# Kernel optimization log

Hardware: AMD Instinct MI355X
Metric: run time of the kernel (lower is better)

The kernel has to match this reference:

```python
import jax, jax.numpy as jnp
import numpy as np
from jax import lax

# --- configuration (matches init_kwargs) ---
NY_I = NX_I = 256      # interior model size
PML = 20               # pml width on each edge
DX = 4.0               # grid spacing (m)
DT = 5e-4              # time step (s); CFL: vmax*DT/DX ~ 0.4 < 0.5
NT = 64                # number of time steps
C1, C2 = 9.0 / 8.0, -1.0 / 24.0   # 4th-order staggered FD coefficients


def _shift(p, axis, off, n):
    idx = [slice(None)] * 3
    idx[axis] = slice(2 + off, 2 + off + n)
    return p[tuple(idx)]


def _dfwd(f, axis):
    # forward (half-cell +) staggered derivative, 4th order, zero halo
    pad = [(0, 0)] * 3
    pad[axis] = (2, 2)
    p = jnp.pad(f, pad)
    n = f.shape[axis]
    return (C1 * (_shift(p, axis, 1, n) - _shift(p, axis, 0, n))
            + C2 * (_shift(p, axis, 2, n) - _shift(p, axis, -1, n))) / DX


def _dbwd(f, axis):
    # backward (half-cell -) staggered derivative, 4th order, zero halo
    pad = [(0, 0)] * 3
    pad[axis] = (2, 2)
    p = jnp.pad(f, pad)
    n = f.shape[axis]
    return (C1 * (_shift(p, axis, 0, n) - _shift(p, axis, -1, n))
            + C2 * (_shift(p, axis, 1, n) - _shift(p, axis, -2, n))) / DX


def _propagate(lamb, mu, buoyancy, amps, src_loc, rec_loc):
    # replicate model edges into the PML region (as deepwave does)
    lambp = jnp.pad(lamb, PML, mode='edge')[None]      # [1,NY,NX]
    mup = jnp.pad(mu, PML, mode='edge')[None]
    buoyp = jnp.pad(buoyancy, PML, mode='edge')[None]
    NY, NX = lambp.shape[1], lambp.shape[2]
    n_shots = amps.shape[0]
    l2m = lambp + 2.0 * mup

    # CPML damping profiles (quadratic), alpha=0, kappa=1
    max_vel = lax.stop_gradient(jnp.max(jnp.sqrt(l2m * buoyp)))
    sig_max = 3.0 * max_vel * jnp.log(1000.0) / (2.0 * PML * DX)

    def prof(n):
        i = jnp.arange(n, dtype=lamb.dtype)
        d = jnp.maximum(jnp.clip(PML - i, 0.0, None),
                        jnp.clip(i - (n - 1 - PML), 0.0, None)) / PML
        return sig_max * d * d

    by = jnp.exp(-prof(NY) * DT)[None, :, None]
    ay = by - 1.0
    bx = jnp.exp(-prof(NX) * DT)[None, None, :]
    ax = bx - 1.0

    shot = jnp.arange(n_shots)[:, None]
    sl = src_loc + PML   # [S,nsrc,2]
    rl = rec_loc + PML   # [S,nrec,2]
    src_b = buoyp[0, sl[..., 0], sl[..., 1]]   # buoyancy at sources [S,nsrc]

    z = jnp.zeros((n_shots, NY, NX), lamb.dtype)
    carry0 = (z,) * 13  # vy,vx,syy,sxy,sxx, m_vyy,m_vyx,m_vxy,m_vxx, m_syyy,m_sxyy,m_sxyx,m_sxxx

    def step(carry, amp_t):
        (vy, vx, syy, sxy, sxx,
         mvyy, mvyx, mvxy, mvxx,
         msyyy, msxyy, msxyx, msxxx) = carry
        # --- velocity update ---
        d = _dbwd(syy, 1); msyyy = by * msyyy + ay * d; dsyy_y = d + msyyy
        d = _dbwd(sxy, 2); msxyx = bx * msxyx + ax * d; dsxy_x = d + msxyx
        vy = vy + DT * buoyp * (dsyy_y + dsxy_x)
        d = _dbwd(sxy, 1); msxyy = by * msxyy + ay * d; dsxy_y = d + msxyy
        d = _dbwd(sxx, 2); msxxx = bx * msxxx + ax * d; dsxx_x = d + msxxx
        vx = vx + DT * buoyp * (dsxy_y + dsxx_x)
        # --- inject y-oriented sources into vy ---
        vy = vy.at[shot, sl[..., 0], sl[..., 1]].add(DT * src_b * amp_t)
        # --- stress update ---
        d = _dfwd(vy, 1); mvyy = by * mvyy + ay * d; dvy_y = d + mvyy
        d = _dfwd(vx, 2); mvxx = bx * mvxx + ax * d; dvx_x = d + mvxx
        syy = syy + DT * (l2m * dvy_y + lambp * dvx_x)
        sxx = sxx + DT * (lambp * dvy_y + l2m * dvx_x)
        d = _dfwd(vy, 2); mvyx = bx * mvyx + ax * d; dvy_x = d + mvyx
        d = _dfwd(vx, 1); mvxy = by * mvxy + ay * d; dvx_y = d + mvxy
        sxy = sxy + DT * mup * (dvy_x + dvx_y)
        # --- record y-oriented receivers ---
        rec = vy[shot, rl[..., 0], rl[..., 1]]   # [S,nrec]
        return ((vy, vx, syy, sxy, sxx,
                 mvyy, mvyx, mvxy, mvxx,
                 msyyy, msxyy, msxyx, msxxx), rec)

    _, recs = lax.scan(step, carry0, jnp.moveaxis(amps, 2, 0))  # recs [nt,S,nrec]
    return jnp.transpose(recs, (1, 2, 0))  # [S,nrec,nt]


def setup_inputs() -> dict:
    key = jax.random.key(0)
    k = jax.random.split(key, 6)
    vp = 3000.0 + 100.0 * jax.random.normal(k[0], (NY_I, NX_I), jnp.float32)
    vs = 1500.0 + 50.0 * jax.random.normal(k[1], (NY_I, NX_I), jnp.float32)
    rho = 2200.0 + 50.0 * jax.random.normal(k[2], (NY_I, NX_I), jnp.float32)
    mu = rho * vs ** 2
    lamb = rho * (vp ** 2 - 2.0 * vs ** 2)
    buoyancy = 1.0 / rho
    source_amplitudes_y = jax.random.normal(k[3], (2, 8, NT), jnp.float32)
    source_locations_y = jax.random.randint(k[4], (2, 8, 2), 0, NY_I)
    receiver_locations_y = jax.random.randint(k[5], (2, 64, 2), 0, NY_I)
    return {
        'lamb': lamb, 'mu': mu, 'buoyancy': buoyancy,
        'source_amplitudes_y': source_amplitudes_y,
        'source_locations_y': source_locations_y,
        'receiver_locations_y': receiver_locations_y,
    }


def reference(lamb, mu, buoyancy, source_amplitudes_y,
              source_locations_y, receiver_locations_y):
    return _propagate(lamb, mu, buoyancy, source_amplitudes_y,
                      source_locations_y, receiver_locations_y)
```

## Files before the change

### kernel.cpp

```cpp
#include <hip/hip_runtime.h>
#include <math.h>

static constexpr int NYI  = 256;
static constexpr int PMLW = 20;
static constexpr int NY   = 296, NX = 296;
static constexpr int NCELL = NY * NX;
static constexpr int NS   = 2;
static constexpr int NSRC = 8;
static constexpr int NREC = 64;
static constexpr int NT   = 64;
static constexpr float DXF = 4.0f;
static constexpr float DTF = 5e-4f;
static constexpr float FC1 = 9.0f / 8.0f;
static constexpr float FC2 = -1.0f / 24.0f;
static constexpr float INV_DX = 1.0f / DXF;

static constexpr int TB = 8, TS = 37;
static constexpr int VS = TS + 4;
static constexpr int SS = TS + 8;
static constexpr int NBLK = TB * TB * NS;
static constexpr int NTHR = 512;
static constexpr int VAREA = VS * VS;
static constexpr int TAREA = TS * TS;
static constexpr int SFRAME = SS * SS - TAREA;
static constexpr int KV = 4, KT = 3;

static constexpr int GSLOT   = 3 * NS * NCELL;
static constexpr int FLG_OFF = 2 * GSLOT;

__device__ __forceinline__ float cohload(const float* p) {
    return __hip_atomic_load(p, __ATOMIC_RELAXED, __HIP_MEMORY_SCOPE_AGENT);
}
__device__ __forceinline__ void cohstore(float* p, float v) {
    __hip_atomic_store(p, v, __ATOMIC_RELAXED, __HIP_MEMORY_SCOPE_AGENT);
}

__global__ __launch_bounds__(NTHR, 1)
void elastic_fused(const float* __restrict__ lamb, const float* __restrict__ mu,
                   const float* __restrict__ buoy, const float* __restrict__ amps,
                   const int* __restrict__ src_loc, const int* __restrict__ rec_loc,
                   float* __restrict__ out, float* __restrict__ ws)
{
    __shared__ float sS[3][SS * SS];
    __shared__ float sV[2][VS * VS];
    __shared__ float byt[VS], ayt[VS], bxt[VS], axt[VS];
    __shared__ float sAmp[NSRC * NT];
    __shared__ float wmax[NTHR / 64];
    __shared__ int   rcnt;
    __shared__ short rl_r[NREC];
    __shared__ int   rl_pos[NREC];

    int* flags = (int*)(ws + FLG_OFF);
    unsigned* gvm = (unsigned*)(flags + NBLK);
    float* gstr = ws;

    const int tid  = threadIdx.x;
    const int shot = blockIdx.x & 1;
    const int tb   = blockIdx.x >> 1;
    const int bty  = tb >> 3, btx = tb & 7;
    const int gy0  = bty * TS, gx0 = btx * TS;
    const int myBlk = blockIdx.x;

    int myNbr = -1;
    if (tid < 8) {
        int idx = tid < 4 ? tid : tid + 1;
        int dy = idx / 3 - 1, dx = idx % 3 - 1;
        int nty = bty + dy, ntx = btx + dx;
        if (nty >= 0 && nty < TB && ntx >= 0 && ntx < TB)
            myNbr = ((nty * TB + ntx) << 1) | shot;
    }

    for (int i = tid; i < 3 * SS * SS; i += NTHR) ((float*)sS)[i] = 0.0f;
    for (int i = tid; i < 2 * VS * VS; i += NTHR) ((float*)sV)[i] = 0.0f;
    if (tid == 0) rcnt = 0;

    {
        int i = myBlk * NTHR + tid;
        float v = (lamb[i] + 2.0f * mu[i]) * buoy[i];
        #pragma unroll
        for (int off = 32; off > 0; off >>= 1)
            v = fmaxf(v, __shfl_down(v, off));
        if ((tid & 63) == 0) wmax[tid >> 6] = v;
    }

    int   sidx_v[KV], vyv[KV], vxv[KV], smk[KV];
    float buo_v[KV];
    float msyyy[KV] = {0,0,0,0}, msxyx[KV] = {0,0,0,0};
    float msxyy[KV] = {0,0,0,0}, msxxx[KV] = {0,0,0,0};
    unsigned cvm = 0, intm = 0;
    #pragma unroll
    for (int k = 0; k < KV; ++k) {
        int vi = tid + NTHR * k;
        bool val = vi < VAREA;
        int vy_ = val ? vi / VS : 0;
        int vx_ = val ? vi - vy_ * VS : 0;
        int gy = gy0 - 2 + vy_, gx = gx0 - 2 + vx_;
        bool ing = val && gy >= 0 && gy < NY && gx >= 0 && gx < NX;
        if (ing) cvm |= 1u << k;
        if (ing && vy_ >= 4 && vy_ <= 37 && vx_ >= 4 && vx_ <= 37) intm |= 1u << k;
        vyv[k] = vy_; vxv[k] = vx_;
        sidx_v[k] = (vy_ + 2) * SS + (vx_ + 2);
        float b = 0.0f;
        if (ing) {
            int iy = min(max(gy - PMLW, 0), NYI - 1);
            int ix = min(max(gx - PMLW, 0), NYI - 1);
            b = buoy[iy * NYI + ix];
        }
        buo_v[k] = b;
        int sm = 0;
        #pragma unroll
        for (int s = 0; s < NSRC; ++s) {
            int sy = src_loc[(shot * NSRC + s) * 2 + 0] + PMLW;
            int sx = src_loc[(shot * NSRC + s) * 2 + 1] + PMLW;
            if (ing && sy == gy && sx == gx) sm |= 1 << s;
        }
        smk[k] = sm;
    }
    const unsigned bndm = cvm & ~intm;

    int   sidx_t[KT], vidx_t[KT], gidx_t[KT], tyt[KT], txt[KT];
    float lam_t[KT], mu_t[KT], l2m_t[KT];
    float mvyy[KT] = {0,0,0}, mvxx[KT] = {0,0,0}, mvyx[KT] = {0,0,0}, mvxy[KT] = {0,0,0};
    unsigned ctm = 0, ringm = 0;
    #pragma unroll
    for (int k = 0; k < KT; ++k) {
        int ti = tid + NTHR * k;
        bool val = ti < TAREA;
        int ty = val ? ti / TS : 0;
        int tx = val ? ti - ty * TS : 0;
        int gy = gy0 + ty, gx = gx0 + tx;
        if (val) ctm |= 1u << k;
        if (val && (ty < 4 || ty >= TS - 4 || tx < 4 || tx >= TS - 4)) ringm |= 1u << k;
        tyt[k] = ty; txt[k] = tx;
        sidx_t[k] = (ty + 4) * SS + (tx + 4);
        vidx_t[k] = (ty + 2) * VS + (tx + 2);
        gidx_t[k] = gy * NX + gx;
        float la = 0.0f, m = 0.0f;
        if (val) {
            int iy = min(max(gy - PMLW, 0), NYI - 1);
            int ix = min(max(gx - PMLW, 0), NYI - 1);
            la = lamb[iy * NYI + ix];
            m  = mu  [iy * NYI + ix];
        }
        lam_t[k] = la; mu_t[k] = m; l2m_t[k] = la + 2.0f * m;
    }

    bool fval[2], fin[2];
    int  flidx[2], fgi[2];
    #pragma unroll
    for (int k = 0; k < 2; ++k) {
        int ff = tid + NTHR * k;
        fval[k] = ff < SFRAME;
        int fy = 0, fx = 0;
        if (fval[k]) {
            if (ff < 4 * SS)      { fy = ff / SS;                 fx = ff - fy * SS; }
            else if (ff < 8 * SS) { int r = ff - 4 * SS; fy = SS - 4 + r / SS; fx = r % SS; }
            else {
                int r = ff - 8 * SS;
                if (r < (SS - 8) * 4) { fy = 4 + (r >> 2); fx = r & 3; }
                else { r -= (SS - 8) * 4; fy = 4 + (r >> 2); fx = SS - 4 + (r & 3); }
            }
        }
        int gy = gy0 - 4 + fy, gx = gx0 - 4 + fx;
        fin[k]   = fval[k] && gy >= 0 && gy < NY && gx >= 0 && gx < NX;
        flidx[k] = fy * SS + fx;
        fgi[k]   = fin[k] ? (gy * NX + gx) : 0;
    }

    __syncthreads();

    if (tid == 0) {
        float v = wmax[0];
        #pragma unroll
        for (int w = 1; w < NTHR / 64; ++w) v = fmaxf(v, wmax[w]);
        __hip_atomic_store(&gvm[myBlk], __float_as_uint(v), __ATOMIC_RELAXED,
                           __HIP_MEMORY_SCOPE_AGENT);
    }
    unsigned* sred = (unsigned*)sAmp;
    if (tid < NBLK) {
        unsigned v;
        for (;;) {
            v = __hip_atomic_load(&gvm[tid], __ATOMIC_RELAXED, __HIP_MEMORY_SCOPE_AGENT);
            if (!(v & 0x80000000u)) break;
            __builtin_amdgcn_s_sleep(1);
        }
        sred[tid] = v;
    }
    __syncthreads();
    if (tid == 0) {
        unsigned mb = sred[0];
        for (int i = 1; i < NBLK; ++i) mb = mb > sred[i] ? mb : sred[i];
        wmax[0] = __uint_as_float(mb);
    }
    __syncthreads();

    const float max_vel = sqrtf(wmax[0]);
    const float sig_max = 3.0f * max_vel * logf(1000.0f) / (2.0f * PMLW * DXF);
    if (tid < VS) {
        auto prof = [&](int g) -> float {
            float fi = (float)g;
            float d1 = fmaxf((float)PMLW - fi, 0.0f);
            float d2 = fmaxf(fi - (float)(NY - 1 - PMLW), 0.0f);
            float dd = fmaxf(d1, d2) * (1.0f / (float)PMLW);
            return expf(-(sig_max * dd * dd) * DTF);
        };
        float b = prof(gy0 - 2 + tid); byt[tid] = b; ayt[tid] = b - 1.0f;
        b = prof(gx0 - 2 + tid);       bxt[tid] = b; axt[tid] = b - 1.0f;
    }
    if (tid < NREC) {
        int r = tid;
        int ry = rec_loc[(shot * NREC + r) * 2 + 0] + PMLW;
        int rx = rec_loc[(shot * NREC + r) * 2 + 1] + PMLW;
        if (ry >= gy0 && ry < gy0 + TS && rx >= gx0 && rx < gx0 + TS) {
            int p = atomicAdd(&rcnt, 1);
            rl_r[p]   = (short)r;
            rl_pos[p] = (ry - gy0 + 2) * VS + (rx - gx0 + 2);
        }
    }
    __syncthreads();
    for (int i = tid; i < NSRC * NT; i += NTHR)
        sAmp[i] = amps[shot * NSRC * NT + i];
    __syncthreads();

    auto do_vel = [&](unsigned m, int t) {
        #pragma unroll
        for (int k = 0; k < KV; ++k) {
            if (!((m >> k) & 1)) continue;
            int si = sidx_v[k];
            float by_ = byt[vyv[k]], ay_ = ayt[vyv[k]];
            float bx_ = bxt[vxv[k]], ax_ = axt[vxv[k]];
            float d, mm;
            d = (FC1 * (sS[0][si] - sS[0][si - SS]) + FC2 * (sS[0][si + SS] - sS[0][si - 2 * SS])) * INV_DX;
            mm = by_ * msyyy[k] + ay_ * d;  msyyy[k] = mm;  float dsyy_y = d + mm;
            d = (FC1 * (sS[1][si] - sS[1][si - 1]) + FC2 * (sS[1][si + 1] - sS[1][si - 2])) * INV_DX;
            mm = bx_ * msxyx[k] + ax_ * d;  msxyx[k] = mm;  float dsxy_x = d + mm;
            d = (FC1 * (sS[1][si] - sS[1][si - SS]) + FC2 * (sS[1][si + SS] - sS[1][si - 2 * SS])) * INV_DX;
            mm = by_ * msxyy[k] + ay_ * d;  msxyy[k] = mm;  float dsxy_y = d + mm;
            d = (FC1 * (sS[2][si] - sS[2][si - 1]) + FC2 * (sS[2][si + 1] - sS[2][si - 2])) * INV_DX;
            mm = bx_ * msxxx[k] + ax_ * d;  msxxx[k] = mm;  float dsxx_x = d + mm;
            int vi = tid + NTHR * k;
            float nvy = sV[0][vi] + DTF * buo_v[k] * (dsyy_y + dsxy_x);
            float nvx = sV[1][vi] + DTF * buo_v[k] * (dsxy_y + dsxx_x);
            if (smk[k]) {
                #pragma unroll
                for (int s = 0; s < NSRC; ++s)
                    if ((smk[k] >> s) & 1) nvy += DTF * buo_v[k] * sAmp[s * NT + t];
            }
            sV[0][vi] = nvy;
            sV[1][vi] = nvx;
        }
    };

    auto do_stress = [&](unsigned m, bool pub, float* gsw) {
        #pragma unroll
        for (int k = 0; k < KT; ++k) {
            if (!((m >> k) & 1)) continue;
            int si = sidx_t[k], vi = vidx_t[k];
            float by_ = byt[tyt[k] + 2], ay_ = ayt[tyt[k] + 2];
            float bx_ = bxt[txt[k] + 2], ax_ = axt[txt[k] + 2];
            float d, mm;
            d = (FC1 * (sV[0][vi + VS] - sV[0][vi]) + FC2 * (sV[0][vi + 2 * VS] - sV[0][vi - VS])) * INV_DX;
            mm = by_ * mvyy[k] + ay_ * d;  mvyy[k] = mm;  float dvy_y = d + mm;
            d = (FC1 * (sV[1][vi + 1] - sV[1][vi]) + FC2 * (sV[1][vi + 2] - sV[1][vi - 1])) * INV_DX;
            mm = bx_ * mvxx[k] + ax_ * d;  mvxx[k] = mm;  float dvx_x = d + mm;
            float nsyy = sS[0][si] + DTF * (l2m_t[k] * dvy_y + lam_t[k] * dvx_x);
            float nsxx = sS[2][si] + DTF * (lam_t[k] * dvy_y + l2m_t[k] * dvx_x);
            d = (FC1 * (sV[0][vi + 1] - sV[0][vi]) + FC2 * (sV[0][vi + 2] - sV[0][vi - 1])) * INV_DX;
            mm = bx_ * mvyx[k] + ax_ * d;  mvyx[k] = mm;  float dvy_x = d + mm;
            d = (FC1 * (sV[1][vi + VS] - sV[1][vi]) + FC2 * (sV[1][vi + 2 * VS] - sV[1][vi - VS])) * INV_DX;
            mm = by_ * mvxy[k] + ay_ * d;  mvxy[k] = mm;  float dvx_y = d + mm;
            float nsxy = sS[1][si] + DTF * mu_t[k] * (dvy_x + dvx_y);
            sS[0][si] = nsyy; sS[1][si] = nsxy; sS[2][si] = nsxx;
            if (pub && ((ringm >> k) & 1)) {
                int gi = gidx_t[k];
                cohstore(&gsw[(0 * NS + shot) * NCELL + gi], nsyy);
                cohstore(&gsw[(1 * NS + shot) * NCELL + gi], nsxy);
                cohstore(&gsw[(2 * NS + shot) * NCELL + gi], nsxx);
            }
        }
    };

    for (int t = 0; t < NT; ++t) {
        const float* gsr = gstr + ((t + 1) & 1) * GSLOT;
        float*       gsw = gstr + (t & 1) * GSLOT;

        do_vel(intm, t);

        if (t > 0 && myNbr >= 0) {
            while (__hip_atomic_load(&flags[myNbr], __ATOMIC_RELAXED,
                                     __HIP_MEMORY_SCOPE_AGENT) < t)
                __builtin_amdgcn_s_sleep(1);
        }
        __syncthreads();

        float fr0[3], fr1[3];
        #pragma unroll
        for (int f = 0; f < 3; ++f) {
            fr0[f] = (t > 0 && fin[0]) ? cohload(&gsr[(f * NS + shot) * NCELL + fgi[0]]) : 0.0f;
            fr1[f] = (t > 0 && fin[1]) ? cohload(&gsr[(f * NS + shot) * NCELL + fgi[1]]) : 0.0f;
        }

        do_stress(ctm & ~ringm, false, gsw);

        if (fval[0]) { sS[0][flidx[0]] = fr0[0]; sS[1][flidx[0]] = fr0[1]; sS[2][flidx[0]] = fr0[2]; }
        if (fval[1]) { sS[0][flidx[1]] = fr1[0]; sS[1][flidx[1]] = fr1[1]; sS[2][flidx[1]] = fr1[2]; }
        __syncthreads();

        do_vel(bndm, t);
        __syncthreads();

        if (tid < rcnt)
            out[(shot * NREC + rl_r[tid]) * NT + t] = sV[0][rl_pos[tid]];

        do_stress(ringm, true, gsw);

        __syncthreads();
        if (tid == 0 && t < NT - 1)
            __hip_atomic_store(&flags[myBlk], t + 1, __ATOMIC_RELAXED,
                               __HIP_MEMORY_SCOPE_AGENT);
    }
}

extern "C" void kernel_launch(void* const* d_in, const int* in_sizes, int n_in,
                              void* d_out, int out_size, void* d_ws, size_t ws_size,
                              hipStream_t stream) {
    const float* lamb    = (const float*)d_in[0];
    const float* mu      = (const float*)d_in[1];
    const float* buoy    = (const float*)d_in[2];
    const float* amps    = (const float*)d_in[3];
    const int*   src_loc = (const int*)d_in[4];
    const int*   rec_loc = (const int*)d_in[5];
    float* ws  = (float*)d_ws;
    float* out = (float*)d_out;

    elastic_fused<<<NBLK, NTHR, 0, stream>>>(lamb, mu, buoy, amps, src_loc, rec_loc, out, ws);
}
```

Before: 330.1 us.

## Split domain into 8x16 rectangular tiles to double persistent block count

```diff
diff --git a/kernel.cpp b/kernel.cpp
--- a/kernel.cpp
+++ b/kernel.cpp
@@ -15,15 +15,17 @@
 static constexpr float FC2 = -1.0f / 24.0f;
 static constexpr float INV_DX = 1.0f / DXF;
 
-static constexpr int TB = 8, TS = 37;
-static constexpr int VS = TS + 4;
-static constexpr int SS = TS + 8;
-static constexpr int NBLK = TB * TB * NS;
+static constexpr int TBY = 8, TBX = 16;
+static constexpr int TSY = 37, TSX = 19;
+static constexpr int VSY = TSY + 4, VSX = TSX + 4;
+static constexpr int SSY = TSY + 8, SSX = TSX + 8;
+static constexpr int VAREA = VSY * VSX;
+static constexpr int SAREA = SSY * SSX;
+static constexpr int TAREA = TSY * TSX;
+static constexpr int SFRAME = SAREA - TAREA;
+static constexpr int NBLK = TBX * TBY * NS;
 static constexpr int NTHR = 512;
-static constexpr int VAREA = VS * VS;
-static constexpr int TAREA = TS * TS;
-static constexpr int SFRAME = SS * SS - TAREA;
-static constexpr int KV = 4, KT = 3;
+static constexpr int KV = 2, KT = 2;
 
 static constexpr int GSLOT   = 3 * NS * NCELL;
 static constexpr int FLG_OFF = 2 * GSLOT;
@@ -41,9 +43,9 @@
                    const int* __restrict__ src_loc, const int* __restrict__ rec_loc,
                    float* __restrict__ out, float* __restrict__ ws)
 {
-    __shared__ float sS[3][SS * SS];
-    __shared__ float sV[2][VS * VS];
-    __shared__ float byt[VS], ayt[VS], bxt[VS], axt[VS];
+    __shared__ float sS[3][SAREA];
+    __shared__ float sV[2][VAREA];
+    __shared__ float byt[VSY], ayt[VSY], bxt[VSX], axt[VSX];
     __shared__ float sAmp[NSRC * NT];
     __shared__ float wmax[NTHR / 64];
     __shared__ int   rcnt;
@@ -57,8 +59,8 @@
     const int tid  = threadIdx.x;
     const int shot = blockIdx.x & 1;
     const int tb   = blockIdx.x >> 1;
-    const int bty  = tb >> 3, btx = tb & 7;
-    const int gy0  = bty * TS, gx0 = btx * TS;
+    const int bty  = tb >> 4, btx = tb & 15;
+    const int gy0  = bty * TSY, gx0 = btx * TSX;
     const int myBlk = blockIdx.x;
 
     int myNbr = -1;
@@ -66,17 +68,20 @@
         int idx = tid < 4 ? tid : tid + 1;
         int dy = idx / 3 - 1, dx = idx % 3 - 1;
         int nty = bty + dy, ntx = btx + dx;
-        if (nty >= 0 && nty < TB && ntx >= 0 && ntx < TB)
-            myNbr = ((nty * TB + ntx) << 1) | shot;
-    }
-
-    for (int i = tid; i < 3 * SS * SS; i += NTHR) ((float*)sS)[i] = 0.0f;
-    for (int i = tid; i < 2 * VS * VS; i += NTHR) ((float*)sV)[i] = 0.0f;
+        if (nty >= 0 && nty < TBY && ntx >= 0 && ntx < TBX)
+            myNbr = ((nty * TBX + ntx) << 1) | shot;
+    }
+
+    for (int i = tid; i < 3 * SAREA; i += NTHR) ((float*)sS)[i] = 0.0f;
+    for (int i = tid; i < 2 * VAREA; i += NTHR) ((float*)sV)[i] = 0.0f;
     if (tid == 0) rcnt = 0;
 
     {
-        int i = myBlk * NTHR + tid;
-        float v = (lamb[i] + 2.0f * mu[i]) * buoy[i];
+        float v = 0.0f;
+        if (tid < 256) {
+            int i = myBlk * 256 + tid;
+            v = (lamb[i] + 2.0f * mu[i]) * buoy[i];
+        }
         #pragma unroll
         for (int off = 32; off > 0; off >>= 1)
             v = fmaxf(v, __shfl_down(v, off));
@@ -85,21 +90,21 @@
 
     int   sidx_v[KV], vyv[KV], vxv[KV], smk[KV];
     float buo_v[KV];
-    float msyyy[KV] = {0,0,0,0}, msxyx[KV] = {0,0,0,0};
-    float msxyy[KV] = {0,0,0,0}, msxxx[KV] = {0,0,0,0};
+    float msyyy[KV] = {0,0}, msxyx[KV] = {0,0};
+    float msxyy[KV] = {0,0}, msxxx[KV] = {0,0};
     unsigned cvm = 0, intm = 0;
     #pragma unroll
     for (int k = 0; k < KV; ++k) {
         int vi = tid + NTHR * k;
         bool val = vi < VAREA;
-        int vy_ = val ? vi / VS : 0;
-        int vx_ = val ? vi - vy_ * VS : 0;
+        int vy_ = val ? vi / VSX : 0;
+        int vx_ = val ? vi - vy_ * VSX : 0;
         int gy = gy0 - 2 + vy_, gx = gx0 - 2 + vx_;
         bool ing = val && gy >= 0 && gy < NY && gx >= 0 && gx < NX;
         if (ing) cvm |= 1u << k;
-        if (ing && vy_ >= 4 && vy_ <= 37 && vx_ >= 4 && vx_ <= 37) intm |= 1u << k;
+        if (ing && vy_ >= 4 && vy_ <= TSY && vx_ >= 4 && vx_ <= TSX) intm |= 1u << k;
         vyv[k] = vy_; vxv[k] = vx_;
-        sidx_v[k] = (vy_ + 2) * SS + (vx_ + 2);
+        sidx_v[k] = (vy_ + 2) * SSX + (vx_ + 2);
         float b = 0.0f;
         if (ing) {
             int iy = min(max(gy - PMLW, 0), NYI - 1);
@@ -120,20 +125,21 @@
 
     int   sidx_t[KT], vidx_t[KT], gidx_t[KT], tyt[KT], txt[KT];
     float lam_t[KT], mu_t[KT], l2m_t[KT];
-    float mvyy[KT] = {0,0,0}, mvxx[KT] = {0,0,0}, mvyx[KT] = {0,0,0}, mvxy[KT] = {0,0,0};
+    float mvyy[KT] = {0,0}, mvxx[KT] = {0,0}, mvyx[KT] = {0,0}, mvxy[KT] = {0,0};
     unsigned ctm = 0, ringm = 0;
     #pragma unroll
     for (int k = 0; k < KT; ++k) {
         int ti = tid + NTHR * k;
-        bool val = ti < TAREA;
-        int ty = val ? ti / TS : 0;
-        int tx = val ? ti - ty * TS : 0;
+        bool v0 = ti < TAREA;
+        int ty = v0 ? ti / TSX : 0;
+        int tx = v0 ? ti - ty * TSX : 0;
         int gy = gy0 + ty, gx = gx0 + tx;
+        bool val = v0 && gx < NX;
         if (val) ctm |= 1u << k;
-        if (val && (ty < 4 || ty >= TS - 4 || tx < 4 || tx >= TS - 4)) ringm |= 1u << k;
+        if (val && (ty < 4 || ty >= TSY - 4 || tx < 4 || tx >= TSX - 4)) ringm |= 1u << k;
         tyt[k] = ty; txt[k] = tx;
-        sidx_t[k] = (ty + 4) * SS + (tx + 4);
-        vidx_t[k] = (ty + 2) * VS + (tx + 2);
+        sidx_t[k] = (ty + 4) * SSX + (tx + 4);
+        vidx_t[k] = (ty + 2) * VSX + (tx + 2);
         gidx_t[k] = gy * NX + gx;
         float la = 0.0f, m = 0.0f;
         if (val) {
@@ -145,26 +151,23 @@
         lam_t[k] = la; mu_t[k] = m; l2m_t[k] = la + 2.0f * m;
     }
 
-    bool fval[2], fin[2];
-    int  flidx[2], fgi[2];
-    #pragma unroll
-    for (int k = 0; k < 2; ++k) {
-        int ff = tid + NTHR * k;
-        fval[k] = ff < SFRAME;
-        int fy = 0, fx = 0;
-        if (fval[k]) {
-            if (ff < 4 * SS)      { fy = ff / SS;                 fx = ff - fy * SS; }
-            else if (ff < 8 * SS) { int r = ff - 4 * SS; fy = SS - 4 + r / SS; fx = r % SS; }
-            else {
-                int r = ff - 8 * SS;
-                if (r < (SS - 8) * 4) { fy = 4 + (r >> 2); fx = r & 3; }
-                else { r -= (SS - 8) * 4; fy = 4 + (r >> 2); fx = SS - 4 + (r & 3); }
-            }
+    bool fin0;
+    int  flidx0, fgi0;
+    {
+        int ff = tid;
+        int fy, fx;
+        if (ff < 4 * SSX)       { fy = ff / SSX;                fx = ff - fy * SSX; }
+        else if (ff < 8 * SSX)  { int r = ff - 4 * SSX; fy = SSY - 4 + r / SSX; fx = r % SSX; }
+        else {
+            int r = ff - 8 * SSX;
+            fy = 4 + (r >> 3);
+            int c = r & 7;
+            fx = c < 4 ? c : (SSX - 8 + c);
         }
         int gy = gy0 - 4 + fy, gx = gx0 - 4 + fx;
-        fin[k]   = fval[k] && gy >= 0 && gy < NY && gx >= 0 && gx < NX;
-        flidx[k] = fy * SS + fx;
-        fgi[k]   = fin[k] ? (gy * NX + gx) : 0;
+        fin0   = gy >= 0 && gy < NY && gx >= 0 && gx < NX;
+        flidx0 = fy * SSX + fx;
+        fgi0   = fin0 ? (gy * NX + gx) : 0;
     }
 
     __syncthreads();
@@ -196,7 +199,7 @@
 
     const float max_vel = sqrtf(wmax[0]);
     const float sig_max = 3.0f * max_vel * logf(1000.0f) / (2.0f * PMLW * DXF);
-    if (tid < VS) {
+    {
         auto prof = [&](int g) -> float {
             float fi = (float)g;
             float d1 = fmaxf((float)PMLW - fi, 0.0f);
@@ -204,17 +207,21 @@
             float dd = fmaxf(d1, d2) * (1.0f / (float)PMLW);
             return expf(-(sig_max * dd * dd) * DTF);
         };
-        float b = prof(gy0 - 2 + tid); byt[tid] = b; ayt[tid] = b - 1.0f;
-        b = prof(gx0 - 2 + tid);       bxt[tid] = b; axt[tid] = b - 1.0f;
+        if (tid < VSY) {
+            float b = prof(gy0 - 2 + tid); byt[tid] = b; ayt[tid] = b - 1.0f;
+        }
+        if (tid < VSX) {
+            float b = prof(gx0 - 2 + tid); bxt[tid] = b; axt[tid] = b - 1.0f;
+        }
     }
     if (tid < NREC) {
         int r = tid;
         int ry = rec_loc[(shot * NREC + r) * 2 + 0] + PMLW;
         int rx = rec_loc[(shot * NREC + r) * 2 + 1] + PMLW;
-        if (ry >= gy0 && ry < gy0 + TS && rx >= gx0 && rx < gx0 + TS) {
+        if (ry >= gy0 && ry < gy0 + TSY && rx >= gx0 && rx < gx0 + TSX) {
             int p = atomicAdd(&rcnt, 1);
             rl_r[p]   = (short)r;
-            rl_pos[p] = (ry - gy0 + 2) * VS + (rx - gx0 + 2);
+            rl_pos[p] = (ry - gy0 + 2) * VSX + (rx - gx0 + 2);
         }
     }
     __syncthreads();
@@ -230,11 +237,11 @@
             float by_ = byt[vyv[k]], ay_ = ayt[vyv[k]];
             float bx_ = bxt[vxv[k]], ax_ = axt[vxv[k]];
             float d, mm;
-            d = (FC1 * (sS[0][si] - sS[0][si - SS]) + FC2 * (sS[0][si + SS] - sS[0][si - 2 * SS])) * INV_DX;
+            d = (FC1 * (sS[0][si] - sS[0][si - SSX]) + FC2 * (sS[0][si + SSX] - sS[0][si - 2 * SSX])) * INV_DX;
             mm = by_ * msyyy[k] + ay_ * d;  msyyy[k] = mm;  float dsyy_y = d + mm;
             d = (FC1 * (sS[1][si] - sS[1][si - 1]) + FC2 * (sS[1][si + 1] - sS[1][si - 2])) * INV_DX;
             mm = bx_ * msxyx[k] + ax_ * d;  msxyx[k] = mm;  float dsxy_x = d + mm;
-            d = (FC1 * (sS[1][si] - sS[1][si - SS]) + FC2 * (sS[1][si + SS] - sS[1][si - 2 * SS])) * INV_DX;
+            d = (FC1 * (sS[1][si] - sS[1][si - SSX]) + FC2 * (sS[1][si + SSX] - sS[1][si - 2 * SSX])) * INV_DX;
             mm = by_ * msxyy[k] + ay_ * d;  msxyy[k] = mm;  float dsxy_y = d + mm;
             d = (FC1 * (sS[2][si] - sS[2][si - 1]) + FC2 * (sS[2][si + 1] - sS[2][si - 2])) * INV_DX;
             mm = bx_ * msxxx[k] + ax_ * d;  msxxx[k] = mm;  float dsxx_x = d + mm;
@@ -259,7 +266,7 @@
             float by_ = byt[tyt[k] + 2], ay_ = ayt[tyt[k] + 2];
             float bx_ = bxt[txt[k] + 2], ax_ = axt[txt[k] + 2];
             float d, mm;
-            d = (FC1 * (sV[0][vi + VS] - sV[0][vi]) + FC2 * (sV[0][vi + 2 * VS] - sV[0][vi - VS])) * INV_DX;
+            d = (FC1 * (sV[0][vi + VSX] - sV[0][vi]) + FC2 * (sV[0][vi + 2 * VSX] - sV[0][vi - VSX])) * INV_DX;
             mm = by_ * mvyy[k] + ay_ * d;  mvyy[k] = mm;  float dvy_y = d + mm;
             d = (FC1 * (sV[1][vi + 1] - sV[1][vi]) + FC2 * (sV[1][vi + 2] - sV[1][vi - 1])) * INV_DX;
             mm = bx_ * mvxx[k] + ax_ * d;  mvxx[k] = mm;  float dvx_x = d + mm;
@@ -267,7 +274,7 @@
             float nsxx = sS[2][si] + DTF * (lam_t[k] * dvy_y + l2m_t[k] * dvx_x);
             d = (FC1 * (sV[0][vi + 1] - sV[0][vi]) + FC2 * (sV[0][vi + 2] - sV[0][vi - 1])) * INV_DX;
             mm = bx_ * mvyx[k] + ax_ * d;  mvyx[k] = mm;  float dvy_x = d + mm;
-            d = (FC1 * (sV[1][vi + VS] - sV[1][vi]) + FC2 * (sV[1][vi + 2 * VS] - sV[1][vi - VS])) * INV_DX;
+            d = (FC1 * (sV[1][vi + VSX] - sV[1][vi]) + FC2 * (sV[1][vi + 2 * VSX] - sV[1][vi - VSX])) * INV_DX;
             mm = by_ * mvxy[k] + ay_ * d;  mvxy[k] = mm;  float dvx_y = d + mm;
             float nsxy = sS[1][si] + DTF * mu_t[k] * (dvy_x + dvx_y);
             sS[0][si] = nsyy; sS[1][si] = nsxy; sS[2][si] = nsxx;
@@ -293,17 +300,14 @@
         }
         __syncthreads();
 
-        float fr0[3], fr1[3];
-        #pragma unroll
-        for (int f = 0; f < 3; ++f) {
-            fr0[f] = (t > 0 && fin[0]) ? cohload(&gsr[(f * NS + shot) * NCELL + fgi[0]]) : 0.0f;
-            fr1[f] = (t > 0 && fin[1]) ? cohload(&gsr[(f * NS + shot) * NCELL + fgi[1]]) : 0.0f;
-        }
+        float fr0[3];
+        #pragma unroll
+        for (int f = 0; f < 3; ++f)
+            fr0[f] = (t > 0 && fin0) ? cohload(&gsr[(f * NS + shot) * NCELL + fgi0]) : 0.0f;
 
         do_stress(ctm & ~ringm, false, gsw);
 
-        if (fval[0]) { sS[0][flidx[0]] = fr0[0]; sS[1][flidx[0]] = fr0[1]; sS[2][flidx[0]] = fr0[2]; }
-        if (fval[1]) { sS[0][flidx[1]] = fr1[0]; sS[1][flidx[1]] = fr1[1]; sS[2][flidx[1]] = fr1[2]; }
+        sS[0][flidx0] = fr0[0]; sS[1][flidx0] = fr0[1]; sS[2][flidx0] = fr0[2];
         __syncthreads();
 
         do_vel(bndm, t);
```

After: 389.7 us. +18.0%, slower.

## Compute four cells per thread with float4 LDS loads and padded tiles

Applied to the files above, without the earlier changes.

```diff
diff --git a/kernel.cpp b/kernel.cpp
--- a/kernel.cpp
+++ b/kernel.cpp
@@ -16,14 +16,13 @@
 static constexpr float INV_DX = 1.0f / DXF;
 
 static constexpr int TB = 8, TS = 37;
-static constexpr int VS = TS + 4;
-static constexpr int SS = TS + 8;
 static constexpr int NBLK = TB * TB * NS;
 static constexpr int NTHR = 512;
-static constexpr int VAREA = VS * VS;
-static constexpr int TAREA = TS * TS;
-static constexpr int SFRAME = SS * SS - TAREA;
-static constexpr int KV = 4, KT = 3;
+static constexpr int SVW = 44, VROWS = 41;
+static constexpr int SSW = 48, SROWS = 45;
+static constexpr int NVINT = 272, NVTOT = 451;
+static constexpr int NSEARLY = 217, NSTOT = 370;
+static constexpr int SFRAME = 656;
 
 static constexpr int GSLOT   = 3 * NS * NCELL;
 static constexpr int FLG_OFF = 2 * GSLOT;
@@ -35,15 +34,25 @@
     __hip_atomic_store(p, v, __ATOMIC_RELAXED, __HIP_MEMORY_SCOPE_AGENT);
 }
 
+__device__ __forceinline__ void ld8(float* __restrict__ dst,
+                                    const float* __restrict__ arr, int idx) {
+    float4 A_ = *(const float4*)&arr[idx];
+    float4 B_ = *(const float4*)&arr[idx + 4];
+    dst[0] = A_.x; dst[1] = A_.y; dst[2] = A_.z; dst[3] = A_.w;
+    dst[4] = B_.x; dst[5] = B_.y; dst[6] = B_.z; dst[7] = B_.w;
+}
+
 __global__ __launch_bounds__(NTHR, 1)
 void elastic_fused(const float* __restrict__ lamb, const float* __restrict__ mu,
                    const float* __restrict__ buoy, const float* __restrict__ amps,
                    const int* __restrict__ src_loc, const int* __restrict__ rec_loc,
                    float* __restrict__ out, float* __restrict__ ws)
 {
-    __shared__ float sS[3][SS * SS];
-    __shared__ float sV[2][VS * VS];
-    __shared__ float byt[VS], ayt[VS], bxt[VS], axt[VS];
+    __shared__ __align__(16) float sSyy[SROWS * SSW];
+    __shared__ __align__(16) float sSxy[SROWS * SSW];
+    __shared__ __align__(16) float sSxx[SROWS * SSW];
+    __shared__ __align__(16) float sVy[VROWS * SVW];
+    __shared__ __align__(16) float sVx[VROWS * SVW];
     __shared__ float sAmp[NSRC * NT];
     __shared__ float wmax[NTHR / 64];
     __shared__ int   rcnt;
@@ -70,8 +79,8 @@
             myNbr = ((nty * TB + ntx) << 1) | shot;
     }
 
-    for (int i = tid; i < 3 * SS * SS; i += NTHR) ((float*)sS)[i] = 0.0f;
-    for (int i = tid; i < 2 * VS * VS; i += NTHR) ((float*)sV)[i] = 0.0f;
+    for (int i = tid; i < SROWS * SSW; i += NTHR) { sSyy[i] = 0.0f; sSxy[i] = 0.0f; sSxx[i] = 0.0f; }
+    for (int i = tid; i < VROWS * SVW; i += NTHR) { sVy[i] = 0.0f; sVx[i] = 0.0f; }
     if (tid == 0) rcnt = 0;
 
     {
@@ -83,66 +92,78 @@
         if ((tid & 63) == 0) wmax[tid >> 6] = v;
     }
 
-    int   sidx_v[KV], vyv[KV], vxv[KV], smk[KV];
-    float buo_v[KV];
-    float msyyy[KV] = {0,0,0,0}, msxyx[KV] = {0,0,0,0};
-    float msxyy[KV] = {0,0,0,0}, msxxx[KV] = {0,0,0,0};
-    unsigned cvm = 0, intm = 0;
+    const bool vact = tid < NVTOT;
+    const bool vint = tid < NVINT;
+    int vrow = 0, vq = 0;
+    if (vint) { vrow = 4 + tid / 8; vq = 1 + (tid & 7); }
+    else if (vact) {
+        int j = tid - NVINT;
+        if (j < 44)      { vrow = j / 11; vq = j % 11; }
+        else if (j < 77) { int k = j - 44; vrow = 38 + k / 11; vq = k % 11; }
+        else             { int k = j - 77; vrow = 4 + k / 3; int c = k % 3;
+                           vq = (c == 0) ? 0 : (c == 1 ? 9 : 10); }
+    }
+    const int c0v = 4 * vq;
+    const int gyv = gy0 - 2 + vrow;
+
+    int sly[NSRC], slx[NSRC];
     #pragma unroll
-    for (int k = 0; k < KV; ++k) {
-        int vi = tid + NTHR * k;
-        bool val = vi < VAREA;
-        int vy_ = val ? vi / VS : 0;
-        int vx_ = val ? vi - vy_ * VS : 0;
-        int gy = gy0 - 2 + vy_, gx = gx0 - 2 + vx_;
-        bool ing = val && gy >= 0 && gy < NY && gx >= 0 && gx < NX;
-        if (ing) cvm |= 1u << k;
-        if (ing && vy_ >= 4 && vy_ <= 37 && vx_ >= 4 && vx_ <= 37) intm |= 1u << k;
-        vyv[k] = vy_; vxv[k] = vx_;
-        sidx_v[k] = (vy_ + 2) * SS + (vx_ + 2);
+    for (int s = 0; s < NSRC; ++s) {
+        sly[s] = src_loc[(shot * NSRC + s) * 2 + 0] + PMLW;
+        slx[s] = src_loc[(shot * NSRC + s) * 2 + 1] + PMLW;
+    }
+
+    int vdm = 0, smk4 = 0;
+    float buo[4];
+    #pragma unroll
+    for (int m = 0; m < 4; ++m) {
+        int vx_ = c0v + m;
+        int gx = gx0 - 2 + vx_;
+        bool ing = vact && vx_ <= 40 && gyv >= 0 && gyv < NY && gx >= 0 && gx < NX;
+        if (ing) vdm |= 1 << m;
         float b = 0.0f;
         if (ing) {
-            int iy = min(max(gy - PMLW, 0), NYI - 1);
+            int iy = min(max(gyv - PMLW, 0), NYI - 1);
             int ix = min(max(gx - PMLW, 0), NYI - 1);
             b = buoy[iy * NYI + ix];
         }
-        buo_v[k] = b;
-        int sm = 0;
-        #pragma unroll
-        for (int s = 0; s < NSRC; ++s) {
-            int sy = src_loc[(shot * NSRC + s) * 2 + 0] + PMLW;
-            int sx = src_loc[(shot * NSRC + s) * 2 + 1] + PMLW;
-            if (ing && sy == gy && sx == gx) sm |= 1 << s;
-        }
-        smk[k] = sm;
-    }
-    const unsigned bndm = cvm & ~intm;
-
-    int   sidx_t[KT], vidx_t[KT], gidx_t[KT], tyt[KT], txt[KT];
-    float lam_t[KT], mu_t[KT], l2m_t[KT];
-    float mvyy[KT] = {0,0,0}, mvxx[KT] = {0,0,0}, mvyx[KT] = {0,0,0}, mvxy[KT] = {0,0,0};
-    unsigned ctm = 0, ringm = 0;
+        buo[m] = b;
+        #pragma unroll
+        for (int s = 0; s < NSRC; ++s)
+            if (ing && sly[s] == gyv && slx[s] == gx) smk4 |= 1 << (m * 8 + s);
+    }
+
+    const bool sact = tid < NSTOT;
+    const bool searly = tid < NSEARLY;
+    int trow = 0, tq = 0;
+    if (searly) { trow = 3 + tid / 7; tq = 1 + tid % 7; }
+    else if (sact) {
+        int j = tid - NSEARLY;
+        if (j < 30)      { trow = j / 10; tq = j % 10; }
+        else if (j < 60) { int k = j - 30; trow = 34 + k / 10; tq = k % 10; }
+        else             { int k = j - 60; trow = 3 + k / 3; int c = k % 3;
+                           tq = (c == 0) ? 0 : (c == 1 ? 8 : 9); }
+    }
+    const int q0 = 4 * tq;
+    const int gys = gy0 + trow;
+    int tmask = 0, rmask = 0;
+    float lam[4], muv[4], l2m[4];
+    int gidx[4];
     #pragma unroll
-    for (int k = 0; k < KT; ++k) {
-        int ti = tid + NTHR * k;
-        bool val = ti < TAREA;
-        int ty = val ? ti / TS : 0;
-        int tx = val ? ti - ty * TS : 0;
-        int gy = gy0 + ty, gx = gx0 + tx;
-        if (val) ctm |= 1u << k;
-        if (val && (ty < 4 || ty >= TS - 4 || tx < 4 || tx >= TS - 4)) ringm |= 1u << k;
-        tyt[k] = ty; txt[k] = tx;
-        sidx_t[k] = (ty + 4) * SS + (tx + 4);
-        vidx_t[k] = (ty + 2) * VS + (tx + 2);
-        gidx_t[k] = gy * NX + gx;
-        float la = 0.0f, m = 0.0f;
+    for (int m = 0; m < 4; ++m) {
+        int tx = q0 + m;
+        bool val = sact && tx <= 36;
+        if (val) tmask |= 1 << m;
+        if (val && (trow < 4 || trow >= TS - 4 || tx < 4 || tx >= TS - 4)) rmask |= 1 << m;
+        gidx[m] = gys * NX + (gx0 + tx);
+        float la = 0.0f, mm_ = 0.0f;
         if (val) {
-            int iy = min(max(gy - PMLW, 0), NYI - 1);
-            int ix = min(max(gx - PMLW, 0), NYI - 1);
+            int iy = min(max(gys - PMLW, 0), NYI - 1);
+            int ix = min(max(gx0 + tx - PMLW, 0), NYI - 1);
             la = lamb[iy * NYI + ix];
-            m  = mu  [iy * NYI + ix];
-        }
-        lam_t[k] = la; mu_t[k] = m; l2m_t[k] = la + 2.0f * m;
+            mm_ = mu[iy * NYI + ix];
+        }
+        lam[m] = la; muv[m] = mm_; l2m[m] = la + 2.0f * mm_;
     }
 
     bool fval[2], fin[2];
@@ -153,17 +174,17 @@
         fval[k] = ff < SFRAME;
         int fy = 0, fx = 0;
         if (fval[k]) {
-            if (ff < 4 * SS)      { fy = ff / SS;                 fx = ff - fy * SS; }
-            else if (ff < 8 * SS) { int r = ff - 4 * SS; fy = SS - 4 + r / SS; fx = r % SS; }
+            if (ff < 4 * SROWS)      { fy = ff / SROWS; fx = ff - fy * SROWS; }
+            else if (ff < 8 * SROWS) { int r = ff - 4 * SROWS; fy = 41 + r / SROWS; fx = r % SROWS; }
             else {
-                int r = ff - 8 * SS;
-                if (r < (SS - 8) * 4) { fy = 4 + (r >> 2); fx = r & 3; }
-                else { r -= (SS - 8) * 4; fy = 4 + (r >> 2); fx = SS - 4 + (r & 3); }
+                int r = ff - 8 * SROWS;
+                if (r < 37 * 4) { fy = 4 + (r >> 2); fx = r & 3; }
+                else { r -= 37 * 4; fy = 4 + (r >> 2); fx = 41 + (r & 3); }
             }
         }
         int gy = gy0 - 4 + fy, gx = gx0 - 4 + fx;
         fin[k]   = fval[k] && gy >= 0 && gy < NY && gx >= 0 && gx < NX;
-        flidx[k] = fy * SS + fx;
+        flidx[k] = fy * SSW + fx;
         fgi[k]   = fin[k] ? (gy * NX + gx) : 0;
     }
 
@@ -196,17 +217,22 @@
 
     const float max_vel = sqrtf(wmax[0]);
     const float sig_max = 3.0f * max_vel * logf(1000.0f) / (2.0f * PMLW * DXF);
-    if (tid < VS) {
-        auto prof = [&](int g) -> float {
-            float fi = (float)g;
-            float d1 = fmaxf((float)PMLW - fi, 0.0f);
-            float d2 = fmaxf(fi - (float)(NY - 1 - PMLW), 0.0f);
-            float dd = fmaxf(d1, d2) * (1.0f / (float)PMLW);
-            return expf(-(sig_max * dd * dd) * DTF);
-        };
-        float b = prof(gy0 - 2 + tid); byt[tid] = b; ayt[tid] = b - 1.0f;
-        b = prof(gx0 - 2 + tid);       bxt[tid] = b; axt[tid] = b - 1.0f;
-    }
+    auto prof = [&](int g) -> float {
+        float fi = (float)g;
+        float d1 = fmaxf((float)PMLW - fi, 0.0f);
+        float d2 = fmaxf(fi - (float)(NY - 1 - PMLW), 0.0f);
+        float dd = fmaxf(d1, d2) * (1.0f / (float)PMLW);
+        return expf(-(sig_max * dd * dd) * DTF);
+    };
+    const float byv = prof(gyv), ayv = byv - 1.0f;
+    const float bys = prof(gys), ays = bys - 1.0f;
+    float bxv[4], axv[4], bxs[4], axs[4];
+    #pragma unroll
+    for (int m = 0; m < 4; ++m) {
+        bxv[m] = prof(gx0 - 2 + c0v + m); axv[m] = bxv[m] - 1.0f;
+        bxs[m] = prof(gx0 + q0 + m);      axs[m] = bxs[m] - 1.0f;
+    }
+
     if (tid < NREC) {
         int r = tid;
         int ry = rec_loc[(shot * NREC + r) * 2 + 0] + PMLW;
@@ -214,7 +240,7 @@
         if (ry >= gy0 && ry < gy0 + TS && rx >= gx0 && rx < gx0 + TS) {
             int p = atomicAdd(&rcnt, 1);
             rl_r[p]   = (short)r;
-            rl_pos[p] = (ry - gy0 + 2) * VS + (rx - gx0 + 2);
+            rl_pos[p] = (ry - gy0 + 2) * SVW + (rx - gx0 + 2);
         }
     }
     __syncthreads();
@@ -222,61 +248,120 @@
         sAmp[i] = amps[shot * NSRC * NT + i];
     __syncthreads();
 
-    auto do_vel = [&](unsigned m, int t) {
-        #pragma unroll
-        for (int k = 0; k < KV; ++k) {
-            if (!((m >> k) & 1)) continue;
-            int si = sidx_v[k];
-            float by_ = byt[vyv[k]], ay_ = ayt[vyv[k]];
-            float bx_ = bxt[vxv[k]], ax_ = axt[vxv[k]];
-            float d, mm;
-            d = (FC1 * (sS[0][si] - sS[0][si - SS]) + FC2 * (sS[0][si + SS] - sS[0][si - 2 * SS])) * INV_DX;
-            mm = by_ * msyyy[k] + ay_ * d;  msyyy[k] = mm;  float dsyy_y = d + mm;
-            d = (FC1 * (sS[1][si] - sS[1][si - 1]) + FC2 * (sS[1][si + 1] - sS[1][si - 2])) * INV_DX;
-            mm = bx_ * msxyx[k] + ax_ * d;  msxyx[k] = mm;  float dsxy_x = d + mm;
-            d = (FC1 * (sS[1][si] - sS[1][si - SS]) + FC2 * (sS[1][si + SS] - sS[1][si - 2 * SS])) * INV_DX;
-            mm = by_ * msxyy[k] + ay_ * d;  msxyy[k] = mm;  float dsxy_y = d + mm;
-            d = (FC1 * (sS[2][si] - sS[2][si - 1]) + FC2 * (sS[2][si + 1] - sS[2][si - 2])) * INV_DX;
-            mm = bx_ * msxxx[k] + ax_ * d;  msxxx[k] = mm;  float dsxx_x = d + mm;
-            int vi = tid + NTHR * k;
-            float nvy = sV[0][vi] + DTF * buo_v[k] * (dsyy_y + dsxy_x);
-            float nvx = sV[1][vi] + DTF * buo_v[k] * (dsxy_y + dsxx_x);
-            if (smk[k]) {
+    float msyyy[4] = {0,0,0,0}, msxyx[4] = {0,0,0,0};
+    float msxyy[4] = {0,0,0,0}, msxxx[4] = {0,0,0,0};
+    float mvyy[4] = {0,0,0,0}, mvxx[4] = {0,0,0,0};
+    float mvyx[4] = {0,0,0,0}, mvxy[4] = {0,0,0,0};
+
+    auto vel_quad = [&](int t) {
+        const int sb = vrow * SSW + c0v;
+        float r0[8], r1[8], r2[8], r3[8];
+        float dsyy_y[4], dsxy_x[4], dsxy_y[4], dsxx_x[4];
+        ld8(r0, sSyy, sb); ld8(r1, sSyy, sb + SSW);
+        ld8(r2, sSyy, sb + 2 * SSW); ld8(r3, sSyy, sb + 3 * SSW);
+        #pragma unroll
+        for (int m = 0; m < 4; ++m)
+            dsyy_y[m] = (FC1 * (r2[m+2] - r1[m+2]) + FC2 * (r3[m+2] - r0[m+2])) * INV_DX;
+        ld8(r0, sSxy, sb); ld8(r1, sSxy, sb + SSW);
+        ld8(r2, sSxy, sb + 2 * SSW); ld8(r3, sSxy, sb + 3 * SSW);
+        #pragma unroll
+        for (int m = 0; m < 4; ++m) {
+            dsxy_y[m] = (FC1 * (r2[m+2] - r1[m+2]) + FC2 * (r3[m+2] - r0[m+2])) * INV_DX;
+            dsxy_x[m] = (FC1 * (r2[m+2] - r2[m+1]) + FC2 * (r2[m+3] - r2[m])) * INV_DX;
+        }
+        ld8(r0, sSxx, sb + 2 * SSW);
+        #pragma unroll
+        for (int m = 0; m < 4; ++m)
+            dsxx_x[m] = (FC1 * (r0[m+2] - r0[m+1]) + FC2 * (r0[m+3] - r0[m])) * INV_DX;
+
+        const int vb = vrow * SVW + c0v;
+        float4 oy4 = *(const float4*)&sVy[vb];
+        float4 ox4 = *(const float4*)&sVx[vb];
+        float ovy[4] = {oy4.x, oy4.y, oy4.z, oy4.w};
+        float ovx[4] = {ox4.x, ox4.y, ox4.z, ox4.w};
+        float nvy[4], nvx[4];
+        #pragma unroll
+        for (int m = 0; m < 4; ++m) {
+            float mm;
+            mm = byv * msyyy[m] + ayv * dsyy_y[m];      msyyy[m] = mm; float dy1 = dsyy_y[m] + mm;
+            mm = bxv[m] * msxyx[m] + axv[m] * dsxy_x[m]; msxyx[m] = mm; float dx1 = dsxy_x[m] + mm;
+            mm = byv * msxyy[m] + ayv * dsxy_y[m];      msxyy[m] = mm; float dy2 = dsxy_y[m] + mm;
+            mm = bxv[m] * msxxx[m] + axv[m] * dsxx_x[m]; msxxx[m] = mm; float dx2 = dsxx_x[m] + mm;
+            nvy[m] = ovy[m] + DTF * buo[m] * (dy1 + dx1);
+            nvx[m] = ovx[m] + DTF * buo[m] * (dy2 + dx2);
+        }
+        if (smk4) {
+            #pragma unroll
+            for (int m = 0; m < 4; ++m) {
                 #pragma unroll
                 for (int s = 0; s < NSRC; ++s)
-                    if ((smk[k] >> s) & 1) nvy += DTF * buo_v[k] * sAmp[s * NT + t];
+                    if ((smk4 >> (m * 8 + s)) & 1) nvy[m] += DTF * buo[m] * sAmp[s * NT + t];
             }
-            sV[0][vi] = nvy;
-            sV[1][vi] = nvx;
+        }
+        if (vdm == 0xF) {
+            *(float4*)&sVy[vb] = make_float4(nvy[0], nvy[1], nvy[2], nvy[3]);
+            *(float4*)&sVx[vb] = make_float4(nvx[0], nvx[1], nvx[2], nvx[3]);
+        } else {
+            #pragma unroll
+            for (int m = 0; m < 4; ++m)
+                if ((vdm >> m) & 1) { sVy[vb + m] = nvy[m]; sVx[vb + m] = nvx[m]; }
         }
     };
 
-    auto do_stress = [&](unsigned m, bool pub, float* gsw) {
-        #pragma unroll
-        for (int k = 0; k < KT; ++k) {
-            if (!((m >> k) & 1)) continue;
-            int si = sidx_t[k], vi = vidx_t[k];
-            float by_ = byt[tyt[k] + 2], ay_ = ayt[tyt[k] + 2];
-            float bx_ = bxt[txt[k] + 2], ax_ = axt[txt[k] + 2];
-            float d, mm;
-            d = (FC1 * (sV[0][vi + VS] - sV[0][vi]) + FC2 * (sV[0][vi + 2 * VS] - sV[0][vi - VS])) * INV_DX;
-            mm = by_ * mvyy[k] + ay_ * d;  mvyy[k] = mm;  float dvy_y = d + mm;
-            d = (FC1 * (sV[1][vi + 1] - sV[1][vi]) + FC2 * (sV[1][vi + 2] - sV[1][vi - 1])) * INV_DX;
-            mm = bx_ * mvxx[k] + ax_ * d;  mvxx[k] = mm;  float dvx_x = d + mm;
-            float nsyy = sS[0][si] + DTF * (l2m_t[k] * dvy_y + lam_t[k] * dvx_x);
-            float nsxx = sS[2][si] + DTF * (lam_t[k] * dvy_y + l2m_t[k] * dvx_x);
-            d = (FC1 * (sV[0][vi + 1] - sV[0][vi]) + FC2 * (sV[0][vi + 2] - sV[0][vi - 1])) * INV_DX;
-            mm = bx_ * mvyx[k] + ax_ * d;  mvyx[k] = mm;  float dvy_x = d + mm;
-            d = (FC1 * (sV[1][vi + VS] - sV[1][vi]) + FC2 * (sV[1][vi + 2 * VS] - sV[1][vi - VS])) * INV_DX;
-            mm = by_ * mvxy[k] + ay_ * d;  mvxy[k] = mm;  float dvx_y = d + mm;
-            float nsxy = sS[1][si] + DTF * mu_t[k] * (dvy_x + dvx_y);
-            sS[0][si] = nsyy; sS[1][si] = nsxy; sS[2][si] = nsxx;
-            if (pub && ((ringm >> k) & 1)) {
-                int gi = gidx_t[k];
-                cohstore(&gsw[(0 * NS + shot) * NCELL + gi], nsyy);
-                cohstore(&gsw[(1 * NS + shot) * NCELL + gi], nsxy);
-                cohstore(&gsw[(2 * NS + shot) * NCELL + gi], nsxx);
-            }
+    auto stress_quad = [&](float* gsw) {
+        const int vb = (trow + 1) * SVW + q0;
+        float y0[8], y1[8], y2[8], y3[8];
+        float dvy_y[4], dvy_x[4], dvx_y[4], dvx_x[4];
+        ld8(y0, sVy, vb); ld8(y1, sVy, vb + SVW);
+        ld8(y2, sVy, vb + 2 * SVW); ld8(y3, sVy, vb + 3 * SVW);
+        #pragma unroll
+        for (int m = 0; m < 4; ++m) {
+            dvy_y[m] = (FC1 * (y2[m+2] - y1[m+2]) + FC2 * (y3[m+2] - y0[m+2])) * INV_DX;
+            dvy_x[m] = (FC1 * (y1[m+3] - y1[m+2]) + FC2 * (y1[m+4] - y1[m+1])) * INV_DX;
+        }
+        ld8(y0, sVx, vb); ld8(y1, sVx, vb + SVW);
+        ld8(y2, sVx, vb + 2 * SVW); ld8(y3, sVx, vb + 3 * SVW);
+        #pragma unroll
+        for (int m = 0; m < 4; ++m) {
+            dvx_x[m] = (FC1 * (y1[m+3] - y1[m+2]) + FC2 * (y1[m+4] - y1[m+1])) * INV_DX;
+            dvx_y[m] = (FC1 * (y2[m+2] - y1[m+2]) + FC2 * (y3[m+2] - y0[m+2])) * INV_DX;
+        }
+        const int sb = (trow + 4) * SSW + q0 + 4;
+        float4 a4 = *(const float4*)&sSyy[sb];
+        float4 b4 = *(const float4*)&sSxy[sb];
+        float4 c4 = *(const float4*)&sSxx[sb];
+        float os0[4] = {a4.x, a4.y, a4.z, a4.w};
+        float os1[4] = {b4.x, b4.y, b4.z, b4.w};
+        float os2[4] = {c4.x, c4.y, c4.z, c4.w};
+        float nsyy[4], nsxy[4], nsxx[4];
+        #pragma unroll
+        for (int m = 0; m < 4; ++m) {
+            float mm;
+            mm = bys * mvyy[m] + ays * dvy_y[m];         mvyy[m] = mm; float fy = dvy_y[m] + mm;
+            mm = bxs[m] * mvxx[m] + axs[m] * dvx_x[m];   mvxx[m] = mm; float fx = dvx_x[m] + mm;
+            nsyy[m] = os0[m] + DTF * (l2m[m] * fy + lam[m] * fx);
+            nsxx[m] = os2[m] + DTF * (lam[m] * fy + l2m[m] * fx);
+            mm = bxs[m] * mvyx[m] + axs[m] * dvy_x[m];   mvyx[m] = mm; float gx_ = dvy_x[m] + mm;
+            mm = bys * mvxy[m] + ays * dvx_y[m];         mvxy[m] = mm; float gy_ = dvx_y[m] + mm;
+            nsxy[m] = os1[m] + DTF * muv[m] * (gx_ + gy_);
+        }
+        if (tmask == 0xF) {
+            *(float4*)&sSyy[sb] = make_float4(nsyy[0], nsyy[1], nsyy[2], nsyy[3]);
+            *(float4*)&sSxy[sb] = make_float4(nsxy[0], nsxy[1], nsxy[2], nsxy[3]);
+            *(float4*)&sSxx[sb] = make_float4(nsxx[0], nsxx[1], nsxx[2], nsxx[3]);
+        } else {
+            #pragma unroll
+            for (int m = 0; m < 4; ++m)
+                if ((tmask >> m) & 1) { sSyy[sb+m] = nsyy[m]; sSxy[sb+m] = nsxy[m]; sSxx[sb+m] = nsxx[m]; }
+        }
+        if (rmask) {
+            #pragma unroll
+            for (int m = 0; m < 4; ++m)
+                if ((rmask >> m) & 1) {
+                    cohstore(&gsw[(0 * NS + shot) * NCELL + gidx[m]], nsyy[m]);
+                    cohstore(&gsw[(1 * NS + shot) * NCELL + gidx[m]], nsxy[m]);
+                    cohstore(&gsw[(2 * NS + shot) * NCELL + gidx[m]], nsxx[m]);
+                }
         }
     };
 
@@ -284,7 +369,7 @@
         const float* gsr = gstr + ((t + 1) & 1) * GSLOT;
         float*       gsw = gstr + (t & 1) * GSLOT;
 
-        do_vel(intm, t);
+        if (vint) vel_quad(t);
 
         if (t > 0 && myNbr >= 0) {
             while (__hip_atomic_load(&flags[myNbr], __ATOMIC_RELAXED,
@@ -300,19 +385,19 @@
             fr1[f] = (t > 0 && fin[1]) ? cohload(&gsr[(f * NS + shot) * NCELL + fgi[1]]) : 0.0f;
         }
 
-        do_stress(ctm & ~ringm, false, gsw);
-
-        if (fval[0]) { sS[0][flidx[0]] = fr0[0]; sS[1][flidx[0]] = fr0[1]; sS[2][flidx[0]] = fr0[2]; }
-        if (fval[1]) { sS[0][flidx[1]] = fr1[0]; sS[1][flidx[1]] = fr1[1]; sS[2][flidx[1]] = fr1[2]; }
+        if (searly) stress_quad(gsw);
+
+        if (fval[0]) { sSyy[flidx[0]] = fr0[0]; sSxy[flidx[0]] = fr0[1]; sSxx[flidx[0]] = fr0[2]; }
+        if (fval[1]) { sSyy[flidx[1]] = fr1[0]; sSxy[flidx[1]] = fr1[1]; sSxx[flidx[1]] = fr1[2]; }
         __syncthreads();
 
-        do_vel(bndm, t);
+        if (vact && !vint) vel_quad(t);
         __syncthreads();
 
         if (tid < rcnt)
-            out[(shot * NREC + rl_r[tid]) * NT + t] = sV[0][rl_pos[tid]];
-
-        do_stress(ringm, true, gsw);
+            out[(shot * NREC + rl_r[tid]) * NT + t] = sVy[rl_pos[tid]];
+
+        if (sact && !searly) stress_quad(gsw);
 
         __syncthreads();
         if (tid == 0 && t < NT - 1)
```

Measured after the change: 505.9 us. +53.2%, slower.
